# Performance work log

Hardware: AMD Instinct MI355X
Metric: run time of the kernel (lower is better)

The kernel has to match this reference:

```python
import jax, jax.numpy as jnp
import numpy as np

EPS = 1e-5
NUM_HEADS = 12
PATCH = 16

def layernorm(x, g, b):
    m = jnp.mean(x, axis=-1, keepdims=True)
    v = jnp.var(x, axis=-1, keepdims=True)
    return (x - m) / jnp.sqrt(v + EPS) * g + b

def setup_inputs() -> dict:
    key = jax.random.key(0)
    ks = jax.random.split(key, 10)
    B, C, H, D, L = 32, 3, 224, 768, 12
    Dff, NCLS = 3072, 5
    N = (H // PATCH) ** 2 + 1  # 197 tokens incl. cls
    def rn(k, shape, s=0.02):
        return jax.random.normal(k, shape, jnp.float32) * s
    return {
        "x": jax.random.normal(ks[0], (B, C, H, H), jnp.float32),
        "conv_w": rn(ks[1], (D, C, PATCH, PATCH)),
        "conv_b": jnp.zeros((D,), jnp.float32),
        "cls_token": rn(ks[2], (1, 1, D)),
        "pos_embed": rn(ks[3], (1, N, D)),
        "ln1_g": jnp.ones((L, D), jnp.float32), "ln1_b": jnp.zeros((L, D), jnp.float32),
        "qkv_w": rn(ks[4], (L, D, 3 * D)), "qkv_b": jnp.zeros((L, 3 * D), jnp.float32),
        "proj_w": rn(ks[5], (L, D, D)), "proj_b": jnp.zeros((L, D), jnp.float32),
        "ln2_g": jnp.ones((L, D), jnp.float32), "ln2_b": jnp.zeros((L, D), jnp.float32),
        "fc1_w": rn(ks[6], (L, D, Dff)), "fc1_b": jnp.zeros((L, Dff), jnp.float32),
        "fc2_w": rn(ks[7], (L, Dff, D)), "fc2_b": jnp.zeros((L, D), jnp.float32),
        "norm_g": jnp.ones((D,), jnp.float32), "norm_b": jnp.zeros((D,), jnp.float32),
        "head_w": rn(ks[8], (D, NCLS)), "head_b": jnp.zeros((NCLS,), jnp.float32),
    }

def reference(x, conv_w, conv_b, cls_token, pos_embed,
              ln1_g, ln1_b, qkv_w, qkv_b, proj_w, proj_b,
              ln2_g, ln2_b, fc1_w, fc1_b, fc2_w, fc2_b,
              norm_g, norm_b, head_w, head_b):
    B = x.shape[0]
    D = conv_w.shape[0]
    HD = D // NUM_HEADS
    scale = HD ** -0.5
    # patch embedding: conv stride=kernel=16 -> [B, D, 14, 14]
    p = jax.lax.conv_general_dilated(
        x, conv_w, (PATCH, PATCH), 'VALID',
        dimension_numbers=('NCHW', 'OIHW', 'NCHW')) + conv_b[None, :, None, None]
    tok = p.reshape(B, D, -1).transpose(0, 2, 1)  # [B, Np, D]
    tok = jnp.concatenate([jnp.broadcast_to(cls_token, (B, 1, D)), tok], axis=1)
    tok = tok + pos_embed  # [B, N, D]; dropout is identity at eval

    def block(h, params):
        l1g, l1b, qw, qb, pw, pb, l2g, l2b, f1w, f1b, f2w, f2b = params
        y = layernorm(h, l1g, l1b)
        qkv = (y @ qw + qb).reshape(B, -1, 3, NUM_HEADS, HD)
        q, k, v = qkv[:, :, 0], qkv[:, :, 1], qkv[:, :, 2]  # [B, N, H, HD]
        attn = jax.nn.softmax(jnp.einsum('bqhd,bkhd->bhqk', q, k) * scale, axis=-1)
        o = jnp.einsum('bhqk,bkhd->bqhd', attn, v).reshape(B, -1, D)
        h = h + (o @ pw + pb)
        y = layernorm(h, l2g, l2b)
        h = h + (jax.nn.gelu(y @ f1w + f1b, approximate=False) @ f2w + f2b)
        return h, None

    tok, _ = jax.lax.scan(
        block, tok,
        (ln1_g, ln1_b, qkv_w, qkv_b, proj_w, proj_b,
         ln2_g, ln2_b, fc1_w, fc1_b, fc2_w, fc2_b))
    cls = layernorm(tok, norm_g, norm_b)[:, 0]  # [B, D]
    return cls @ head_w + head_b  # [B, num_classes]
```

## Files before the change

kernel.cpp:

```cpp
#include <hip/hip_runtime.h>
#include <hip/hip_bf16.h>
#include <math.h>

#define B_      32
#define NTOK    197
#define NPATCH  196
#define D_      768
#define DFF     3072
#define L_      12
#define NH      12
#define HD      64
#define NCLS    5
#define MTOK    (B_ * NTOK)
#define MPAD    6400
#define MPATCH  (B_ * NPATCH)
#define KPAD    224
#define KS_STR  72
#define VT_STR  232

typedef __attribute__((ext_vector_type(8))) short short8;
typedef __attribute__((ext_vector_type(4))) float floatx4;

static __device__ inline short f2bf(float f) {
  __hip_bfloat16 h = __float2bfloat16(f);
  short s; __builtin_memcpy(&s, &h, 2); return s;
}

__global__ __launch_bounds__(256) void cls_pos_kernel(
    const float* __restrict__ cls, const float* __restrict__ pos,
    float* __restrict__ tok) {
  int i = blockIdx.x * 256 + threadIdx.x;
  if (i < B_ * D_) {
    int b = i / D_, d = i % D_;
    tok[(size_t)b * NTOK * D_ + d] = cls[d] + pos[d];
  }
}

__global__ __launch_bounds__(256) void cvt_kernel(
    const float* __restrict__ src, short* __restrict__ dst, int n) {
  int i = blockIdx.x * 256 + threadIdx.x;
  if (i < n) dst[i] = f2bf(src[i]);
}

__global__ __launch_bounds__(256) void wconv_kernel(
    const float* __restrict__ W, short* __restrict__ Wt, int K, int N) {
  __shared__ float t[32][33];
  int n0 = blockIdx.x * 32, k0 = blockIdx.y * 32;
  int tid = threadIdx.x;
#pragma unroll
  for (int q = 0; q < 4; q++) {
    int e = q * 256 + tid;
    int rk = e >> 5, cn = e & 31;
    t[rk][cn] = W[(size_t)(k0 + rk) * N + n0 + cn];
  }
  __syncthreads();
#pragma unroll
  for (int q = 0; q < 4; q++) {
    int e = q * 256 + tid;
    int rn = e >> 5, ck = e & 31;
    Wt[(size_t)(n0 + rn) * K + k0 + ck] = f2bf(t[ck][rn]);
  }
}

__global__ __launch_bounds__(256) void im2col_kernel(
    const float* __restrict__ x, short* __restrict__ Abf) {
  int i = blockIdx.x * 256 + threadIdx.x;
  if (i >= MPATCH * D_) return;
  int row = i / D_, col = i % D_;
  int b = row / NPATCH, n = row % NPATCH;
  int ph = n / 14, pw = n % 14;
  int c = col >> 8, r = col & 255;
  int kh = r >> 4, kw = r & 15;
  Abf[i] = f2bf(x[(((size_t)b * 3 + c) * 224 + (ph * 16 + kh)) * 224 + (pw * 16 + kw)]);
}

__global__ __launch_bounds__(256) void patch_scatter_kernel(
    const float* __restrict__ po, const float* __restrict__ pos,
    float* __restrict__ tok) {
  int i = blockIdx.x * 256 + threadIdx.x;
  if (i >= MPATCH * D_) return;
  int row = i / D_, col = i % D_;
  int b = row / NPATCH, n = row % NPATCH;
  tok[((size_t)b * NTOK + 1 + n) * D_ + col] = po[i] + pos[(size_t)(1 + n) * D_ + col];
}

template <bool OBF>
__global__ __launch_bounds__(256) void ln_kernel(
    const float* __restrict__ in, void* __restrict__ out,
    const float* __restrict__ g, const float* __restrict__ bt,
    long rs_in) {
  int row = blockIdx.x;
  const float* xr = in + (size_t)row * rs_in;
  int tid = threadIdx.x;
  float v0 = xr[tid], v1 = xr[tid + 256], v2 = xr[tid + 512];
  float s = v0 + v1 + v2;
#pragma unroll
  for (int off = 32; off; off >>= 1) s += __shfl_xor(s, off);
  __shared__ float red1[4], red2[4];
  int wid = tid >> 6, lane = tid & 63;
  if (lane == 0) red1[wid] = s;
  __syncthreads();
  float mean = (red1[0] + red1[1] + red1[2] + red1[3]) * (1.f / 768.f);
  float d0 = v0 - mean, d1 = v1 - mean, d2 = v2 - mean;
  float s2 = d0 * d0 + d1 * d1 + d2 * d2;
#pragma unroll
  for (int off = 32; off; off >>= 1) s2 += __shfl_xor(s2, off);
  if (lane == 0) red2[wid] = s2;
  __syncthreads();
  float var = (red2[0] + red2[1] + red2[2] + red2[3]) * (1.f / 768.f);
  float rstd = rsqrtf(var + 1e-5f);
  float o0 = d0 * rstd * g[tid]       + bt[tid];
  float o1 = d1 * rstd * g[tid + 256] + bt[tid + 256];
  float o2 = d2 * rstd * g[tid + 512] + bt[tid + 512];
  if (OBF) {
    short* yr = (short*)out + (size_t)row * D_;
    yr[tid] = f2bf(o0); yr[tid + 256] = f2bf(o1); yr[tid + 512] = f2bf(o2);
  } else {
    float* yr = (float*)out + (size_t)row * D_;
    yr[tid] = o0; yr[tid + 256] = o1; yr[tid + 512] = o2;
  }
}

template <bool OBF, bool RES, bool GELU_>
__global__ __launch_bounds__(256) void gemm_bf16_kernel(
    const short* __restrict__ A, const short* __restrict__ Wt,
    const float* __restrict__ bias, const float* __restrict__ res,
    void* __restrict__ Cout, int M, int N, int K) {
  __shared__ short As[128 * 32];
  __shared__ short Bs[128 * 32];
  const int tid = threadIdx.x;
  const int lane = tid & 63;
  const int wid = tid >> 6;
  const int wave_m = wid >> 1, wave_n = wid & 1;
  const int mbase = blockIdx.y * 128;
  const int nbase = blockIdx.x * 128;

  const int lrow = lane >> 2;
  const int kbg = (lane & 3) ^ ((lane >> 3) & 3);
  const short* ga0 = A + (size_t)(mbase + wid * 32 + lrow) * K + kbg * 8;
  const short* ga1 = A + (size_t)(mbase + wid * 32 + 16 + lrow) * K + kbg * 8;
  const short* gb0 = Wt + (size_t)(nbase + wid * 32 + lrow) * K + kbg * 8;
  const short* gb1 = Wt + (size_t)(nbase + wid * 32 + 16 + lrow) * K + kbg * 8;
  typedef const __attribute__((address_space(1))) unsigned* gp_t;
  typedef __attribute__((address_space(3))) unsigned* lp_t;
  lp_t lA0 = (lp_t)(void*)(As + wid * 1024);
  lp_t lA1 = (lp_t)(void*)(As + wid * 1024 + 512);
  lp_t lB0 = (lp_t)(void*)(Bs + wid * 1024);
  lp_t lB1 = (lp_t)(void*)(Bs + wid * 1024 + 512);

  floatx4 zero = {0.f, 0.f, 0.f, 0.f};
  floatx4 acc[4][4];
#pragma unroll
  for (int i = 0; i < 4; i++)
#pragma unroll
    for (int j = 0; j < 4; j++) acc[i][j] = zero;

  const int quad = lane >> 4;
  const int l15 = lane & 15;
  const int s = quad ^ ((l15 >> 1) & 3);

  for (int k0 = 0; k0 < K; k0 += 32) {
    __builtin_amdgcn_global_load_lds((gp_t)(const void*)ga0, lA0, 16, 0, 0);
    __builtin_amdgcn_global_load_lds((gp_t)(const void*)ga1, lA1, 16, 0, 0);
    __builtin_amdgcn_global_load_lds((gp_t)(const void*)gb0, lB0, 16, 0, 0);
    __builtin_amdgcn_global_load_lds((gp_t)(const void*)gb1, lB1, 16, 0, 0);
    ga0 += 32; ga1 += 32; gb0 += 32; gb1 += 32;
    __syncthreads();
    short8 a[4], b[4];
#pragma unroll
    for (int i = 0; i < 4; i++) {
      int r = wave_m * 64 + i * 16 + l15;
      a[i] = *(const short8*)(As + r * 32 + s * 8);
      int c = wave_n * 64 + i * 16 + l15;
      b[i] = *(const short8*)(Bs + c * 32 + s * 8);
    }
#pragma unroll
    for (int i = 0; i < 4; i++)
#pragma unroll
      for (int j = 0; j < 4; j++)
        acc[i][j] = __builtin_amdgcn_mfma_f32_16x16x32_bf16(a[i], b[j], acc[i][j], 0, 0, 0);
    __syncthreads();
  }

#pragma unroll
  for (int i = 0; i < 4; i++) {
    int gm0 = mbase + wave_m * 64 + i * 16 + quad * 4;
#pragma unroll
    for (int r = 0; r < 4; r++) {
      int gm = gm0 + r;
      if (gm >= M) continue;
#pragma unroll
      for (int j = 0; j < 4; j++) {
        int gn = nbase + wave_n * 64 + j * 16 + l15;
        float c = acc[i][j][r] + bias[gn];
        if (RES) c += res[(size_t)gm * N + gn];
        if (GELU_) c = 0.5f * c * (1.f + erff(c * 0.70710678118654752f));
        if (OBF) ((short*)Cout)[(size_t)gm * N + gn] = f2bf(c);
        else ((float*)Cout)[(size_t)gm * N + gn] = c;
      }
    }
  }
}

__global__ __launch_bounds__(256) void attn_mfma_kernel(
    const short* __restrict__ qkv, short* __restrict__ o) {
  __shared__ short Ks[KPAD * KS_STR];
  __shared__ short Vt[64 * VT_STR];
  __shared__ short Pw[4 * 16 * VT_STR];
  const int h = blockIdx.x % NH;
  const int b = blockIdx.x / NH;
  const int tid = threadIdx.x;
  const int lane = tid & 63, wid = tid >> 6;
  const size_t rowbase = (size_t)b * NTOK * (3 * D_);

  for (int it = 0; it < 7; it++) {
    int idx = it * 256 + tid;
    int dblk = idx / KPAD, key = idx % KPAD;
    int krow = key < NTOK ? key : NTOK - 1;
    const short* src = qkv + rowbase + (size_t)krow * (3 * D_) + h * HD;
    short8 kv = *(const short8*)(src + D_ + dblk * 8);
    *(short8*)(Ks + key * KS_STR + dblk * 8) = kv;
    short8 vv = *(const short8*)(src + 2 * D_ + dblk * 8);
#pragma unroll
    for (int i = 0; i < 8; i++) Vt[(dblk * 8 + i) * VT_STR + key] = vv[i];
  }
  __syncthreads();

  const int quad = lane >> 4, l15 = lane & 15;
  short* P = Pw + wid * 16 * VT_STR;
  const floatx4 zero = {0.f, 0.f, 0.f, 0.f};

  for (int qt = wid; qt < 14; qt += 4) {
    int qrow = qt * 16 + l15;
    int qr = qrow < NTOK ? qrow : NTOK - 1;
    const short* qbase = qkv + rowbase + (size_t)qr * (3 * D_) + h * HD;
    short8 a0 = *(const short8*)(qbase + quad * 8);
    short8 a1 = *(const short8*)(qbase + 32 + quad * 8);

    floatx4 s[14];
#pragma unroll
    for (int kt = 0; kt < 14; kt++) {
      const short* kb = Ks + (kt * 16 + l15) * KS_STR;
      short8 b0 = *(const short8*)(kb + quad * 8);
      short8 b1 = *(const short8*)(kb + 32 + quad * 8);
      floatx4 c = __builtin_amdgcn_mfma_f32_16x16x32_bf16(a0, b0, zero, 0, 0, 0);
      s[kt] = __builtin_amdgcn_mfma_f32_16x16x32_bf16(a1, b1, c, 0, 0, 0);
    }
#pragma unroll
    for (int kt = 0; kt < 14; kt++) {
      if (kt * 16 + l15 >= NTOK) {
#pragma unroll
        for (int r = 0; r < 4; r++) s[kt][r] = -1e30f;
      }
    }
    float mx[4] = {-1e30f, -1e30f, -1e30f, -1e30f};
#pragma unroll
    for (int kt = 0; kt < 14; kt++)
#pragma unroll
      for (int r = 0; r < 4; r++) mx[r] = fmaxf(mx[r], s[kt][r]);
#pragma unroll
    for (int off = 1; off < 16; off <<= 1)
#pragma unroll
      for (int r = 0; r < 4; r++) mx[r] = fmaxf(mx[r], __shfl_xor(mx[r], off));
    float lsum[4] = {0.f, 0.f, 0.f, 0.f};
#pragma unroll
    for (int kt = 0; kt < 14; kt++) {
#pragma unroll
      for (int r = 0; r < 4; r++) {
        float p = __expf(0.125f * (s[kt][r] - mx[r]));
        lsum[r] += p;
        P[(quad * 4 + r) * VT_STR + kt * 16 + l15] = f2bf(p);
      }
    }
#pragma unroll
    for (int off = 1; off < 16; off <<= 1)
#pragma unroll
      for (int r = 0; r < 4; r++) lsum[r] += __shfl_xor(lsum[r], off);
    float inv[4];
#pragma unroll
    for (int r = 0; r < 4; r++) inv[r] = 1.f / lsum[r];

    floatx4 oacc[4] = {zero, zero, zero, zero};
#pragma unroll
    for (int kk = 0; kk < 7; kk++) {
      short8 a = *(const short8*)(P + l15 * VT_STR + kk * 32 + quad * 8);
#pragma unroll
      for (int nt = 0; nt < 4; nt++) {
        short8 bv = *(const short8*)(Vt + (nt * 16 + l15) * VT_STR + kk * 32 + quad * 8);
        oacc[nt] = __builtin_amdgcn_mfma_f32_16x16x32_bf16(a, bv, oacc[nt], 0, 0, 0);
      }
    }
#pragma unroll
    for (int r = 0; r < 4; r++) {
      int q = qt * 16 + quad * 4 + r;
      if (q >= NTOK) continue;
      short* orow = o + ((size_t)(b * NTOK + q)) * D_ + h * HD;
#pragma unroll
      for (int nt = 0; nt < 4; nt++)
        orow[nt * 16 + l15] = f2bf(oacc[nt][r] * inv[r]);
    }
  }
}

__global__ __launch_bounds__(64) void head_kernel(
    const float* __restrict__ y, const float* __restrict__ hw,
    const float* __restrict__ hb, float* __restrict__ out) {
  int b = blockIdx.x;
  const float* yr = y + (size_t)b * D_;
  int lane = threadIdx.x;
  for (int j = 0; j < NCLS; j++) {
    float s = 0.f;
    for (int d = lane; d < D_; d += 64) s += yr[d] * hw[(size_t)d * NCLS + j];
#pragma unroll
    for (int off = 32; off; off >>= 1) s += __shfl_xor(s, off);
    if (lane == 0) out[b * NCLS + j] = s + hb[j];
  }
}

extern "C" void kernel_launch(void* const* d_in, const int* in_sizes, int n_in,
                              void* d_out, int out_size, void* d_ws, size_t ws_size,
                              hipStream_t stream) {
  const float* x        = (const float*)d_in[0];
  const float* conv_w   = (const float*)d_in[1];
  const float* conv_b   = (const float*)d_in[2];
  const float* cls_tok  = (const float*)d_in[3];
  const float* pos_emb  = (const float*)d_in[4];
  const float* ln1_g    = (const float*)d_in[5];
  const float* ln1_b    = (const float*)d_in[6];
  const float* qkv_w    = (const float*)d_in[7];
  const float* qkv_b    = (const float*)d_in[8];
  const float* proj_w   = (const float*)d_in[9];
  const float* proj_b   = (const float*)d_in[10];
  const float* ln2_g    = (const float*)d_in[11];
  const float* ln2_b    = (const float*)d_in[12];
  const float* fc1_w    = (const float*)d_in[13];
  const float* fc1_b    = (const float*)d_in[14];
  const float* fc2_w    = (const float*)d_in[15];
  const float* fc2_b    = (const float*)d_in[16];
  const float* norm_g   = (const float*)d_in[17];
  const float* norm_b   = (const float*)d_in[18];
  const float* head_w   = (const float*)d_in[19];
  const float* head_b   = (const float*)d_in[20];
  float* out = (float*)d_out;

  char* p = (char*)d_ws;
  float* tok    = (float*)p;                 p += (size_t)MTOK * D_ * 4;
  short* y_bf   = (short*)p;                 p += (size_t)MPAD * D_ * 2;
  short* o_bf   = (short*)p;                 p += (size_t)MPAD * D_ * 2;
  short* h_bf   = (short*)p;                 p += (size_t)MPAD * DFF * 2;
  short* wt_qkv = (short*)p;                 p += (size_t)D_ * 3 * D_ * 2;
  short* wt_prj = (short*)p;                 p += (size_t)D_ * D_ * 2;
  short* wt_fc1 = (short*)p;                 p += (size_t)D_ * DFF * 2;
  short* wt_fc2 = (short*)p;                 p += (size_t)DFF * D_ * 2;
  short* cw_bf  = (short*)p;                 p += (size_t)D_ * D_ * 2;
  short* im_bf  = (short*)p;                 p += (size_t)MPAD * D_ * 2;
  float* big1   = (float*)p;                 p += (size_t)MTOK * 3 * D_ * 4;
  short* qkv_bf = (short*)big1;
  float* pout   = big1;
  float* yf     = (float*)(p);

  cvt_kernel<<<(D_ * D_ + 255) / 256, 256, 0, stream>>>(conv_w, cw_bf, D_ * D_);
  im2col_kernel<<<(MPATCH * D_ + 255) / 256, 256, 0, stream>>>(x, im_bf);
  cls_pos_kernel<<<(B_ * D_ + 255) / 256, 256, 0, stream>>>(cls_tok, pos_emb, tok);
  {
    dim3 g(D_ / 128, (MPATCH + 127) / 128);
    gemm_bf16_kernel<false, false, false><<<g, 256, 0, stream>>>(
        im_bf, cw_bf, conv_b, nullptr, pout, MPATCH, D_, D_);
  }
  patch_scatter_kernel<<<(MPATCH * D_ + 255) / 256, 256, 0, stream>>>(pout, pos_emb, tok);

  dim3 gQKV(3 * D_ / 128, (MTOK + 127) / 128);
  dim3 gPRJ(D_ / 128, (MTOK + 127) / 128);
  dim3 gFC1(DFF / 128, (MTOK + 127) / 128);
  dim3 gFC2(D_ / 128, (MTOK + 127) / 128);

  for (int l = 0; l < L_; l++) {
    const float* l1g = ln1_g + l * D_;
    const float* l1b = ln1_b + l * D_;
    const float* qw  = qkv_w + (size_t)l * D_ * 3 * D_;
    const float* qb  = qkv_b + (size_t)l * 3 * D_;
    const float* pw  = proj_w + (size_t)l * D_ * D_;
    const float* pb  = proj_b + (size_t)l * D_;
    const float* l2g = ln2_g + l * D_;
    const float* l2b = ln2_b + l * D_;
    const float* f1w = fc1_w + (size_t)l * D_ * DFF;
    const float* f1b = fc1_b + (size_t)l * DFF;
    const float* f2w = fc2_w + (size_t)l * DFF * D_;
    const float* f2b = fc2_b + (size_t)l * D_;

    { dim3 g(3 * D_ / 32, D_ / 32);  wconv_kernel<<<g, 256, 0, stream>>>(qw, wt_qkv, D_, 3 * D_); }
    { dim3 g(D_ / 32, D_ / 32);      wconv_kernel<<<g, 256, 0, stream>>>(pw, wt_prj, D_, D_); }
    { dim3 g(DFF / 32, D_ / 32);     wconv_kernel<<<g, 256, 0, stream>>>(f1w, wt_fc1, D_, DFF); }
    { dim3 g(D_ / 32, DFF / 32);     wconv_kernel<<<g, 256, 0, stream>>>(f2w, wt_fc2, DFF, D_); }

    ln_kernel<true><<<MTOK, 256, 0, stream>>>(tok, y_bf, l1g, l1b, D_);
    gemm_bf16_kernel<true, false, false><<<gQKV, 256, 0, stream>>>(
        y_bf, wt_qkv, qb, nullptr, qkv_bf, MTOK, 3 * D_, D_);
    attn_mfma_kernel<<<B_ * NH, 256, 0, stream>>>(qkv_bf, o_bf);
    gemm_bf16_kernel<false, true, false><<<gPRJ, 256, 0, stream>>>(
        o_bf, wt_prj, pb, tok, tok, MTOK, D_, D_);
    ln_kernel<true><<<MTOK, 256, 0, stream>>>(tok, y_bf, l2g, l2b, D_);
    gemm_bf16_kernel<true, false, true><<<gFC1, 256, 0, stream>>>(
        y_bf, wt_fc1, f1b, nullptr, h_bf, MTOK, DFF, D_);
    gemm_bf16_kernel<false, true, false><<<gFC2, 256, 0, stream>>>(
        h_bf, wt_fc2, f2b, tok, tok, MTOK, D_, DFF);
  }

  ln_kernel<false><<<B_, 256, 0, stream>>>(tok, yf, norm_g, norm_b, (long)NTOK * D_);
  head_kernel<<<B_, 64, 0, stream>>>(yf, head_w, head_b, out);
}
```

Baseline: 3.798 ms.

## Double-buffer GEMM LDS tiles, use 64-row tiles for narrow GEMMs, fuse weight conversion

The bf16 MFMA GEMM now keeps two LDS buffers. It issues the global-to-LDS loads for the next K slice before the MFMAs on the current one, which drops one barrier per iteration and lets loads overlap compute. A BM=64 variant with 128 threads is used for the N=768 GEMMs (patch embed, proj, fc2) to raise the block count and improve CU fill. The four per-layer weight transpose/convert launches are merged into one kernel to cut launch overhead. In exchange, LDS use doubles and the smaller tiles reuse data less.

```diff
diff --git a/kernel.cpp b/kernel.cpp
--- a/kernel.cpp
+++ b/kernel.cpp
@@ -42,23 +42,33 @@
   if (i < n) dst[i] = f2bf(src[i]);
 }
 
-__global__ __launch_bounds__(256) void wconv_kernel(
-    const float* __restrict__ W, short* __restrict__ Wt, int K, int N) {
-  __shared__ float t[32][33];
-  int n0 = blockIdx.x * 32, k0 = blockIdx.y * 32;
+__global__ __launch_bounds__(256) void wconv_all_kernel(
+    const float* __restrict__ qw, const float* __restrict__ pw,
+    const float* __restrict__ f1w, const float* __restrict__ f2w,
+    short* __restrict__ wq, short* __restrict__ wp,
+    short* __restrict__ w1, short* __restrict__ w2) {
+  int id = blockIdx.x;
+  const float* W; short* Wt; int K, N, t;
+  if (id < 1728)      { W = qw;  Wt = wq; K = 768;  N = 2304; t = id; }
+  else if (id < 2304) { W = pw;  Wt = wp; K = 768;  N = 768;  t = id - 1728; }
+  else if (id < 4608) { W = f1w; Wt = w1; K = 768;  N = 3072; t = id - 2304; }
+  else                { W = f2w; Wt = w2; K = 3072; N = 768;  t = id - 4608; }
+  int ntn = N >> 5;
+  int k0 = (t / ntn) * 32, n0 = (t % ntn) * 32;
+  __shared__ float tt[32][33];
   int tid = threadIdx.x;
 #pragma unroll
   for (int q = 0; q < 4; q++) {
     int e = q * 256 + tid;
     int rk = e >> 5, cn = e & 31;
-    t[rk][cn] = W[(size_t)(k0 + rk) * N + n0 + cn];
+    tt[rk][cn] = W[(size_t)(k0 + rk) * N + n0 + cn];
   }
   __syncthreads();
 #pragma unroll
   for (int q = 0; q < 4; q++) {
     int e = q * 256 + tid;
     int rn = e >> 5, ck = e & 31;
-    Wt[(size_t)(n0 + rn) * K + k0 + ck] = f2bf(t[ck][rn]);
+    Wt[(size_t)(n0 + rn) * K + k0 + ck] = f2bf(tt[ck][rn]);
   }
 }
 
@@ -121,32 +131,43 @@
   }
 }
 
-template <bool OBF, bool RES, bool GELU_>
-__global__ __launch_bounds__(256) void gemm_bf16_kernel(
+template <int BM, bool OBF, bool RES, bool GELU_>
+__global__ __launch_bounds__(256) void gemm_db_kernel(
     const short* __restrict__ A, const short* __restrict__ Wt,
     const float* __restrict__ bias, const float* __restrict__ res,
     void* __restrict__ Cout, int M, int N, int K) {
-  __shared__ short As[128 * 32];
-  __shared__ short Bs[128 * 32];
+  constexpr int NBI = (BM == 128) ? 2 : 4;
+  __shared__ short As[2][BM * 32];
+  __shared__ short Bs[2][128 * 32];
   const int tid = threadIdx.x;
   const int lane = tid & 63;
   const int wid = tid >> 6;
-  const int wave_m = wid >> 1, wave_n = wid & 1;
-  const int mbase = blockIdx.y * 128;
+  const int wave_m = (BM == 128) ? (wid >> 1) : 0;
+  const int wave_n = (BM == 128) ? (wid & 1) : wid;
+  const int mbase = blockIdx.y * BM;
   const int nbase = blockIdx.x * 128;
 
   const int lrow = lane >> 2;
   const int kbg = (lane & 3) ^ ((lane >> 3) & 3);
-  const short* ga0 = A + (size_t)(mbase + wid * 32 + lrow) * K + kbg * 8;
-  const short* ga1 = A + (size_t)(mbase + wid * 32 + 16 + lrow) * K + kbg * 8;
-  const short* gb0 = Wt + (size_t)(nbase + wid * 32 + lrow) * K + kbg * 8;
-  const short* gb1 = Wt + (size_t)(nbase + wid * 32 + 16 + lrow) * K + kbg * 8;
+
+  const short* gA0 = A + (size_t)(mbase + wid * 32 + lrow) * K + kbg * 8;
+  const short* gA1 = gA0 + 16 * (size_t)K;
+  const int brow0 = (BM == 128) ? (wid * 32) : (wid * 64);
+  const short* gB[NBI];
+  gB[0] = Wt + (size_t)(nbase + brow0 + lrow) * K + kbg * 8;
+#pragma unroll
+  for (int c = 1; c < NBI; c++) gB[c] = gB[0] + (size_t)c * 16 * K;
+
   typedef const __attribute__((address_space(1))) unsigned* gp_t;
   typedef __attribute__((address_space(3))) unsigned* lp_t;
-  lp_t lA0 = (lp_t)(void*)(As + wid * 1024);
-  lp_t lA1 = (lp_t)(void*)(As + wid * 1024 + 512);
-  lp_t lB0 = (lp_t)(void*)(Bs + wid * 1024);
-  lp_t lB1 = (lp_t)(void*)(Bs + wid * 1024 + 512);
+  const int aoff = wid * 1024;
+  const int boff = brow0 * 32;
+
+  __builtin_amdgcn_global_load_lds((gp_t)(const void*)gA0, (lp_t)(void*)(&As[0][aoff]), 16, 0, 0);
+  __builtin_amdgcn_global_load_lds((gp_t)(const void*)gA1, (lp_t)(void*)(&As[0][aoff + 512]), 16, 0, 0);
+#pragma unroll
+  for (int c = 0; c < NBI; c++)
+    __builtin_amdgcn_global_load_lds((gp_t)(const void*)gB[c], (lp_t)(void*)(&Bs[0][boff + c * 512]), 16, 0, 0);
 
   floatx4 zero = {0.f, 0.f, 0.f, 0.f};
   floatx4 acc[4][4];
@@ -159,27 +180,29 @@
   const int l15 = lane & 15;
   const int s = quad ^ ((l15 >> 1) & 3);
 
-  for (int k0 = 0; k0 < K; k0 += 32) {
-    __builtin_amdgcn_global_load_lds((gp_t)(const void*)ga0, lA0, 16, 0, 0);
-    __builtin_amdgcn_global_load_lds((gp_t)(const void*)ga1, lA1, 16, 0, 0);
-    __builtin_amdgcn_global_load_lds((gp_t)(const void*)gb0, lB0, 16, 0, 0);
-    __builtin_amdgcn_global_load_lds((gp_t)(const void*)gb1, lB1, 16, 0, 0);
-    ga0 += 32; ga1 += 32; gb0 += 32; gb1 += 32;
+  const int niter = K >> 5;
+  for (int it = 0; it < niter; it++) {
+    const int cur = it & 1, nxt = cur ^ 1;
     __syncthreads();
+    if (it + 1 < niter) {
+      const int ks = (it + 1) << 5;
+      __builtin_amdgcn_global_load_lds((gp_t)(const void*)(gA0 + ks), (lp_t)(void*)(&As[nxt][aoff]), 16, 0, 0);
+      __builtin_amdgcn_global_load_lds((gp_t)(const void*)(gA1 + ks), (lp_t)(void*)(&As[nxt][aoff + 512]), 16, 0, 0);
+#pragma unroll
+      for (int c = 0; c < NBI; c++)
+        __builtin_amdgcn_global_load_lds((gp_t)(const void*)(gB[c] + ks), (lp_t)(void*)(&Bs[nxt][boff + c * 512]), 16, 0, 0);
+    }
     short8 a[4], b[4];
 #pragma unroll
     for (int i = 0; i < 4; i++) {
-      int r = wave_m * 64 + i * 16 + l15;
-      a[i] = *(const short8*)(As + r * 32 + s * 8);
-      int c = wave_n * 64 + i * 16 + l15;
-      b[i] = *(const short8*)(Bs + c * 32 + s * 8);
+      a[i] = *(const short8*)(&As[cur][(wave_m * 64 + i * 16 + l15) * 32 + s * 8]);
+      b[i] = *(const short8*)(&Bs[cur][(wave_n * 64 + i * 16 + l15) * 32 + s * 8]);
     }
 #pragma unroll
     for (int i = 0; i < 4; i++)
 #pragma unroll
       for (int j = 0; j < 4; j++)
         acc[i][j] = __builtin_amdgcn_mfma_f32_16x16x32_bf16(a[i], b[j], acc[i][j], 0, 0, 0);
-    __syncthreads();
   }
 
 #pragma unroll
@@ -363,16 +386,16 @@
   im2col_kernel<<<(MPATCH * D_ + 255) / 256, 256, 0, stream>>>(x, im_bf);
   cls_pos_kernel<<<(B_ * D_ + 255) / 256, 256, 0, stream>>>(cls_tok, pos_emb, tok);
   {
-    dim3 g(D_ / 128, (MPATCH + 127) / 128);
-    gemm_bf16_kernel<false, false, false><<<g, 256, 0, stream>>>(
+    dim3 g(D_ / 128, MPATCH / 64);
+    gemm_db_kernel<64, false, false, false><<<g, 128, 0, stream>>>(
         im_bf, cw_bf, conv_b, nullptr, pout, MPATCH, D_, D_);
   }
   patch_scatter_kernel<<<(MPATCH * D_ + 255) / 256, 256, 0, stream>>>(pout, pos_emb, tok);
 
   dim3 gQKV(3 * D_ / 128, (MTOK + 127) / 128);
-  dim3 gPRJ(D_ / 128, (MTOK + 127) / 128);
+  dim3 gPRJ(D_ / 128, (MTOK + 63) / 64);
   dim3 gFC1(DFF / 128, (MTOK + 127) / 128);
-  dim3 gFC2(D_ / 128, (MTOK + 127) / 128);
+  dim3 gFC2(D_ / 128, (MTOK + 63) / 64);
 
   for (int l = 0; l < L_; l++) {
     const float* l1g = ln1_g + l * D_;
@@ -388,21 +411,19 @@
     const float* f2w = fc2_w + (size_t)l * DFF * D_;
     const float* f2b = fc2_b + (size_t)l * D_;
 
-    { dim3 g(3 * D_ / 32, D_ / 32);  wconv_kernel<<<g, 256, 0, stream>>>(qw, wt_qkv, D_, 3 * D_); }
-    { dim3 g(D_ / 32, D_ / 32);      wconv_kernel<<<g, 256, 0, stream>>>(pw, wt_prj, D_, D_); }
-    { dim3 g(DFF / 32, D_ / 32);     wconv_kernel<<<g, 256, 0, stream>>>(f1w, wt_fc1, D_, DFF); }
-    { dim3 g(D_ / 32, DFF / 32);     wconv_kernel<<<g, 256, 0, stream>>>(f2w, wt_fc2, DFF, D_); }
+    wconv_all_kernel<<<6912, 256, 0, stream>>>(qw, pw, f1w, f2w,
+                                               wt_qkv, wt_prj, wt_fc1, wt_fc2);
 
     ln_kernel<true><<<MTOK, 256, 0, stream>>>(tok, y_bf, l1g, l1b, D_);
-    gemm_bf16_kernel<true, false, false><<<gQKV, 256, 0, stream>>>(
+    gemm_db_kernel<128, true, false, false><<<gQKV, 256, 0, stream>>>(
         y_bf, wt_qkv, qb, nullptr, qkv_bf, MTOK, 3 * D_, D_);
     attn_mfma_kernel<<<B_ * NH, 256, 0, stream>>>(qkv_bf, o_bf);
-    gemm_bf16_kernel<false, true, false><<<gPRJ, 256, 0, stream>>>(
+    gemm_db_kernel<64, false, true, false><<<gPRJ, 128, 0, stream>>>(
         o_bf, wt_prj, pb, tok, tok, MTOK, D_, D_);
     ln_kernel<true><<<MTOK, 256, 0, stream>>>(tok, y_bf, l2g, l2b, D_);
-    gemm_bf16_kernel<true, false, true><<<gFC1, 256, 0, stream>>>(
+    gemm_db_kernel<128, true, false, true><<<gFC1, 256, 0, stream>>>(
         y_bf, wt_fc1, f1b, nullptr, h_bf, MTOK, DFF, D_);
-    gemm_bf16_kernel<false, true, false><<<gFC2, 256, 0, stream>>>(
+    gemm_db_kernel<64, false, true, false><<<gFC2, 128, 0, stream>>>(
         h_bf, wt_fc2, f2b, tok, tok, MTOK, D_, DFF);
   }
 
```

Result: faster. 3.686 ms (-3.0%).
